# Performance work log

Hardware: AMD Instinct MI355X
Metric: run time of the kernel (lower is better)

Reference implementation:

```python
import jax, jax.numpy as jnp
import numpy as np
from jax import lax

ITERATIONS = 1000
DK_LEN = 32
STATE = 32  # hash state size in bytes


def _simple_hmac(key, message):
    """Faithful port of Model._simple_hmac.

    Absorb loop: result[i%32] = (result[i%32]*31 + combined[i]) & 255
      (note Python precedence: '*'/'+' bind tighter than '&').
    Mix loop (4x32, sequential in-place updates):
      result[i] = (result[i] ^ (result[(i+17)%32] + result[(i+11)%32])) & 255
      ('+' binds tighter than '^', '&' binds loosest).
    Both loops carry a serial dependency, expressed as lax.scan over the state.
    """
    combined = jnp.concatenate([key, message])
    idx = jnp.arange(combined.shape[0]) % STATE

    def absorb(r, ci):
        c, i = ci
        return r.at[i].set((r[i] * 31 + c) & 255), None

    r0 = jnp.zeros(STATE, dtype=combined.dtype)
    r, _ = lax.scan(absorb, r0, (combined, idx))

    mix_idx = jnp.tile(jnp.arange(STATE), 4)  # 4 rounds x 32 positions, in order

    def mix(r, i):
        v = (r[i] ^ (r[(i + 17) % STATE] + r[(i + 11) % STATE])) & 255
        return r.at[i].set(v), None

    r, _ = lax.scan(mix, r, mix_idx)
    return r


def setup_inputs() -> dict:
    key = jax.random.key(0)
    k1, k2 = jax.random.split(key)
    password = jax.random.randint(k1, (16,), 0, 256, dtype=jnp.int32)
    salt = jax.random.randint(k2, (16,), 0, 256, dtype=jnp.int32)
    return {"password": password, "salt": salt}


def reference(password, salt):
    num_blocks = (DK_LEN + 31) // STATE  # = 1 for dk_len=32
    blocks = []
    for block_idx in range(num_blocks):
        block_num = jnp.array([0, 0, 0, block_idx + 1], dtype=password.dtype)
        U0 = _simple_hmac(password, jnp.concatenate([salt, block_num]))

        def pbkdf2_iter(carry, _):
            U, F = carry
            U = _simple_hmac(password, U)
            return (U, F ^ U), None

        (_, F), _ = lax.scan(pbkdf2_iter, (U0, U0), None, length=ITERATIONS - 1)
        blocks.append(F)
    return jnp.concatenate(blocks)[:DK_LEN]
```

## Files before the change

kernel.cpp:

```cpp
#include <hip/hip_runtime.h>


template<bool FLIP>
__device__ __forceinline__ void run_chain(unsigned &u, unsigned &v,
                                          unsigned &Fu, unsigned &Fv,
                                          unsigned p31v,
                                          bool j_ge11, bool m_le13,
                                          bool m_le14, bool m_s15)
{
    constexpr int P1  = FLIP ? 0x121 : 0x12F;
    constexpr int P11 = FLIP ? 0x12B : 0x125;

#define D1(w)  ((unsigned)__builtin_amdgcn_mov_dpp((int)(w), P1,  0xF, 0xF, false))
#define D11(w) ((unsigned)__builtin_amdgcn_mov_dpp((int)(w), P11, 0xF, 0xF, false))
#define SB()   __builtin_amdgcn_sched_barrier(0)

#define MIXROUND                                                   \
  { unsigned w1   = j_ge11 ? u : v;          SB();                 \
    unsigned w3   = m_s15 ? u : v;           SB();                 \
    unsigned A1   = D1(v);                   SB();                 \
    unsigned g11a = D11(w1);                 SB();                 \
    unsigned nu1  = u ^ (A1 + g11a);         SB();                 \
    unsigned w2   = j_ge11 ? v : nu1;        SB();                 \
    unsigned A2   = D1(nu1);                 SB();                 \
    unsigned G    = D11(w2);                 SB();                 \
    unsigned Gm   = m_s15 ? g11a : G;        SB();                 \
    unsigned m_   = w3 ^ (A2 + Gm);          SB();                 \
    u = m_le14 ? nu1 : m_;                   SB();                 \
    unsigned g17c = D1(m_);                  SB();                 \
    unsigned nv3  = v ^ (g17c + G);                                \
    v = m_le13 ? m_ : nv3;                   SB();                 \
  }

    MIXROUND; MIXROUND; MIXROUND; MIXROUND;

    Fu = u; Fv = v;

    #pragma unroll 3
    for (int it = 0; it < 999; ++it) {
        unsigned nu = v + p31v;
        v = u;
        u = nu;
        SB();
        MIXROUND; MIXROUND; MIXROUND; MIXROUND;
        Fu ^= u;
        Fv ^= v;
        SB();
    }

#undef MIXROUND
#undef SB
#undef D11
#undef D1
}

__global__ void __launch_bounds__(64) Model_62955630625117_kernel(
    const int* __restrict__ pw_g,
    const int* __restrict__ salt_g,
    int* __restrict__ out)
{
    const int lane = (int)threadIdx.x;
    const unsigned s = (unsigned)(lane & 15);

    const bool j_ge11 = (s >= 11u);
    const bool m_le13 = (s <= 13u);
    const bool m_le14 = (s <= 14u);
    const bool m_s15  = (s == 15u);

    int q = __builtin_amdgcn_mov_dpp((int)s, 0x12F, 0xF, 0xF, false);
    const bool dppflip = (__builtin_amdgcn_readfirstlane(q) != 1);

    const unsigned pwv  = (unsigned)pw_g[s];
    const unsigned p31v = pwv * 31u;

    unsigned u = (s < 4u) ? (p31v + (s == 3u ? 1u : 0u)) : pwv;
    unsigned v = (unsigned)salt_g[s];

    unsigned Fu, Fv;
    if (dppflip) run_chain<true >(u, v, Fu, Fv, p31v, j_ge11, m_le13, m_le14, m_s15);
    else         run_chain<false>(u, v, Fu, Fv, p31v, j_ge11, m_le13, m_le14, m_s15);

    if (lane < 32) out[lane] = (int)((lane < 16 ? Fu : Fv) & 255u);
}

extern "C" void kernel_launch(void* const* d_in, const int* in_sizes, int n_in,
                              void* d_out, int out_size, void* d_ws, size_t ws_size,
                              hipStream_t stream) {
    const int* pw   = (const int*)d_in[0];
    const int* salt = (const int*)d_in[1];
    int* out = (int*)d_out;
    Model_62955630625117_kernel<<<1, 64, 0, stream>>>(pw, salt, out);
}
```

Measured before the change: 144.5 us.

## Software-pipeline mix rounds across iterations, hoisting next-round DPP operands early

Restructures the serial mix chain so each round precomputes the next round's first DPP shuffles (A1, g11a, w3) inside the current round, shortening the critical dependency path per round. The iteration boundary is folded into the last round, with the absorb step (u = v + p31, swap) pre-applied to the hoisted operands using lane-masked p31 offsets. The F accumulation XORs are deferred into slack slots of later rounds. This adds extra masks and selects and relies on tricky lane-wise algebra that must exactly match the original sequential semantics.

```diff
diff --git a/kernel.cpp b/kernel.cpp
--- a/kernel.cpp
+++ b/kernel.cpp
@@ -2,11 +2,12 @@
 
 
 template<bool FLIP>
-__device__ __forceinline__ void run_chain(unsigned &u, unsigned &v,
+__device__ __forceinline__ void run_chain(unsigned &u_, unsigned &v_,
                                           unsigned &Fu, unsigned &Fv,
-                                          unsigned p31v,
-                                          bool j_ge11, bool m_le13,
-                                          bool m_le14, bool m_s15)
+                                          unsigned p31v, unsigned p31m, unsigned p31s,
+                                          bool j_ge11, bool m_le13, bool m_le14,
+                                          bool m_s15, bool m_s14, bool m_1114,
+                                          bool m_1314)
 {
     constexpr int P1  = FLIP ? 0x121 : 0x12F;
     constexpr int P11 = FLIP ? 0x12B : 0x125;
@@ -15,40 +16,77 @@
 #define D11(w) ((unsigned)__builtin_amdgcn_mov_dpp((int)(w), P11, 0xF, 0xF, false))
 #define SB()   __builtin_amdgcn_sched_barrier(0)
 
-#define MIXROUND                                                   \
-  { unsigned w1   = j_ge11 ? u : v;          SB();                 \
-    unsigned w3   = m_s15 ? u : v;           SB();                 \
-    unsigned A1   = D1(v);                   SB();                 \
-    unsigned g11a = D11(w1);                 SB();                 \
-    unsigned nu1  = u ^ (A1 + g11a);         SB();                 \
-    unsigned w2   = j_ge11 ? v : nu1;        SB();                 \
-    unsigned A2   = D1(nu1);                 SB();                 \
-    unsigned G    = D11(w2);                 SB();                 \
-    unsigned Gm   = m_s15 ? g11a : G;        SB();                 \
-    unsigned m_   = w3 ^ (A2 + Gm);          SB();                 \
-    u = m_le14 ? nu1 : m_;                   SB();                 \
-    unsigned g17c = D1(m_);                  SB();                 \
-    unsigned nv3  = v ^ (g17c + G);                                \
-    v = m_le13 ? m_ : nv3;                   SB();                 \
-  }
+    unsigned u = u_, v = v_;
+    unsigned w1h, g11ah, w3h, A1h;
+    unsigned uFp = 0u, vFp = 0u;
+    Fu = 0u; Fv = 0u;
 
-    MIXROUND; MIXROUND; MIXROUND; MIXROUND;
+    w1h = j_ge11 ? u : v;
+    w3h = m_s15 ? u : v;
+    A1h = D1(v);
+    g11ah = D11(w1h);
 
-    Fu = u; Fv = v;
+#define MID(FILL)                                               \
+  { unsigned t1   = A1h + g11ah;             SB();              \
+    unsigned nu1  = u ^ t1;                  SB();              \
+    unsigned w2   = j_ge11 ? v : nu1;        SB();              \
+    FILL;                                    SB();              \
+    unsigned A2   = D1(nu1);                 SB();              \
+    unsigned G    = D11(w2);                 SB();              \
+    unsigned Gm   = m_s15 ? g11ah : G;       SB();              \
+    unsigned t2   = A2 + Gm;                 SB();              \
+    unsigned m_   = w3h ^ t2;                SB();              \
+    w1h = m_1114 ? nu1 : m_;                 SB();              \
+    u   = m_le14 ? nu1 : m_;                 SB();              \
+    unsigned g17c = D1(m_);                  SB();              \
+    g11ah = D11(w1h);                        SB();              \
+    unsigned t3   = g17c + G;                SB();              \
+    unsigned nv3  = v ^ t3;                  SB();              \
+    unsigned vm   = m_le13 ? m_ : nv3;       SB();              \
+    w3h = m_s14 ? nv3 : m_;                  SB();              \
+    unsigned D1x  = D1(nv3);                 SB();              \
+    A1h = m_1314 ? D1x : g17c;               SB();              \
+    v = vm; }
 
-    #pragma unroll 3
-    for (int it = 0; it < 999; ++it) {
-        unsigned nu = v + p31v;
-        v = u;
-        u = nu;
-        SB();
-        MIXROUND; MIXROUND; MIXROUND; MIXROUND;
-        Fu ^= u;
-        Fv ^= v;
-        SB();
+#define BOUNDARY                                                \
+  { unsigned t1   = A1h + g11ah;             SB();              \
+    unsigned nu1  = u ^ t1;                  SB();              \
+    unsigned w2   = j_ge11 ? v : nu1;        SB();              \
+    ((void)0);                               SB();              \
+    unsigned A2   = D1(nu1);                 SB();              \
+    unsigned G    = D11(w2);                 SB();              \
+    unsigned Gm   = m_s15 ? g11ah : G;       SB();              \
+    unsigned t2   = A2 + Gm;                 SB();              \
+    unsigned m_   = w3h ^ t2;                SB();              \
+    unsigned uF   = m_le14 ? nu1 : m_;       SB();              \
+    ((void)0);                               SB();              \
+    unsigned g17c = D1(m_);                  SB();              \
+    A1h = D1(uF);                            SB();              \
+    unsigned t3   = g17c + G;                SB();              \
+    unsigned nv3  = v ^ t3;                  SB();              \
+    unsigned vF   = m_le13 ? m_ : nv3;       SB();              \
+    unsigned cndx = j_ge11 ? vF : uF;        SB();              \
+    unsigned w1n  = cndx + p31m;             SB();              \
+    unsigned sx   = m_s15 ? vF : uF;         SB();              \
+    w3h = sx + p31s;                         SB();              \
+    g11ah = D11(w1n);                        SB();              \
+    w1h = w1n;                                                  \
+    u = vF + p31v;                           SB();              \
+    v = uF;                                                     \
+    uFp = uF; vFp = vF; }
+
+    #pragma unroll 1
+    for (int b = 0; b < 1000; ++b) {
+        MID(Fu ^= uFp);
+        MID(Fv ^= vFp);
+        MID(((void)0));
+        BOUNDARY;
     }
+    Fu ^= uFp;
+    Fv ^= vFp;
 
-#undef MIXROUND
+#undef BOUNDARY
+#undef MID
 #undef SB
 #undef D11
 #undef D1
@@ -66,19 +104,26 @@
     const bool m_le13 = (s <= 13u);
     const bool m_le14 = (s <= 14u);
     const bool m_s15  = (s == 15u);
+    const bool m_s14  = (s == 14u);
+    const bool m_1114 = (s >= 11u) & (s <= 14u);
+    const bool m_1314 = (s >= 13u) & (s <= 14u);
 
     int q = __builtin_amdgcn_mov_dpp((int)s, 0x12F, 0xF, 0xF, false);
     const bool dppflip = (__builtin_amdgcn_readfirstlane(q) != 1);
 
     const unsigned pwv  = (unsigned)pw_g[s];
     const unsigned p31v = pwv * 31u;
+    const unsigned p31m = j_ge11 ? p31v : 0u;
+    const unsigned p31s = m_s15  ? p31v : 0u;
 
     unsigned u = (s < 4u) ? (p31v + (s == 3u ? 1u : 0u)) : pwv;
     unsigned v = (unsigned)salt_g[s];
 
     unsigned Fu, Fv;
-    if (dppflip) run_chain<true >(u, v, Fu, Fv, p31v, j_ge11, m_le13, m_le14, m_s15);
-    else         run_chain<false>(u, v, Fu, Fv, p31v, j_ge11, m_le13, m_le14, m_s15);
+    if (dppflip) run_chain<true >(u, v, Fu, Fv, p31v, p31m, p31s,
+                                  j_ge11, m_le13, m_le14, m_s15, m_s14, m_1114, m_1314);
+    else         run_chain<false>(u, v, Fu, Fv, p31v, p31m, p31s,
+                                  j_ge11, m_le13, m_le14, m_s15, m_s14, m_1114, m_1314);
 
     if (lane < 32) out[lane] = (int)((lane < 16 ? Fu : Fv) & 255u);
 }
```

New measurement: 155.9 us. 7.9% more time.
